# Kernel optimization log

Hardware: AMD Instinct MI355X
Metric: run time of the kernel (lower is better)

## Reference

```python
import jax, jax.numpy as jnp
import numpy as np
from jax import lax

N_QUBITS = 8
N_BLOCKS = 5

_H = jnp.array([[1.0, 1.0], [1.0, -1.0]], dtype=jnp.complex64) / np.sqrt(2.0).astype(np.float32)
# torchquantum PauliY.diagonalizing_gates = [Z, S, H] applied in order -> matrix H @ S @ Z = H @ diag(1, -1j)
_YROT = _H @ jnp.diag(jnp.array([1.0, -1j], dtype=jnp.complex64))


def apply_gate(st, U, wires):
    # st: [N, 2, 2, ..., 2] (n_qubits trailing axes); U: [2^k, 2^k]
    k = len(wires)
    axes = [w + 1 for w in wires]
    s = jnp.moveaxis(st, axes, list(range(1, k + 1)))
    shp = s.shape
    s = s.reshape(shp[0], 2 ** k, -1)
    s = jnp.einsum('ij,bjr->bir', U, s)
    return jnp.moveaxis(s.reshape(shp), list(range(1, k + 1)), axes)


def u3_mat(th, ph, lam):
    c = jnp.cos(0.5 * th).astype(jnp.complex64)
    s = jnp.sin(0.5 * th).astype(jnp.complex64)
    el = jnp.exp(1j * lam)
    ep = jnp.exp(1j * ph)
    return jnp.stack([jnp.stack([c, -el * s]), jnp.stack([ep * s, ep * el * c])])


def cu3_mat(th, ph, lam):
    M = jnp.eye(4, dtype=jnp.complex64)
    return M.at[2:, 2:].set(u3_mat(th, ph, lam))


def z_expvals(st):
    # <Z_w> for every wire from marginal probabilities
    n = st.ndim - 1
    mag = st.real ** 2 + st.imag ** 2
    outs = []
    for w in range(n):
        axes = tuple(a for a in range(1, n + 1) if a != w + 1)
        p = mag.sum(axes)  # [N, 2]
        outs.append(p[:, 0] - p[:, 1])
    return jnp.stack(outs, axis=1)


def quantum_conv(x, conv_w, conv_b, u3_params, cu3_params, fc_w, fc_b):
    n = N_QUBITS
    B, C, H, W = x.shape
    y = lax.conv_general_dilated(x, conv_w, (1, 1), 'SAME',
                                 dimension_numbers=('NCHW', 'OIHW', 'NCHW'))
    y = y + conv_b[None, :, None, None]
    ang = y.transpose(0, 2, 3, 1).reshape(-1, n)  # [B*H*W, n_qubits]
    Npx = ang.shape[0]
    # RY(theta)|0> encoding: product state of [cos(t/2), sin(t/2)] per wire
    c = jnp.cos(0.5 * ang)
    s = jnp.sin(0.5 * ang)
    st = jnp.stack([c[:, 0], s[:, 0]], axis=1).astype(jnp.complex64)
    for w in range(1, n):
        q = jnp.stack([c[:, w], s[:, w]], axis=1).astype(jnp.complex64)
        st = (st[:, :, None] * q[:, None, :]).reshape(Npx, -1)
    st = st.reshape((Npx,) + (2,) * n)
    # U3CU3Layer0: per block, U3 on each wire then circular CU3 ring
    for b in range(N_BLOCKS):
        for w in range(n):
            st = apply_gate(st, u3_mat(u3_params[b, w, 0], u3_params[b, w, 1], u3_params[b, w, 2]), [w])
        for w in range(n):
            st = apply_gate(st, cu3_mat(cu3_params[b, w, 0], cu3_params[b, w, 1], cu3_params[b, w, 2]), [w, (w + 1) % n])
    # MeasureAll(Z), then MeasureAll(X) and MeasureAll(Y) which MUTATE the device
    # state with their diagonalizing gates (torchquantum semantics)
    mz = z_expvals(st)
    for w in range(n):
        st = apply_gate(st, _H, [w])
    mx = z_expvals(st)
    for w in range(n):
        st = apply_gate(st, _YROT, [w])
    my = z_expvals(st)
    meas = jnp.concatenate([mz, mx, my], axis=1)  # [B*H*W, 3*n]
    out = meas @ fc_w.T + fc_b
    return out.reshape(B, H, W, -1).transpose(0, 3, 1, 2)


def setup_inputs() -> dict:
    key = jax.random.key(0)
    ks = jax.random.split(key, 7)
    n, cin, cout = N_QUBITS, 16, 32
    x = jax.random.normal(ks[0], (4, cin, 64, 64), dtype=jnp.float32)
    conv_w = jax.random.normal(ks[1], (n, cin, 3, 3), dtype=jnp.float32) / np.sqrt(cin * 9)
    conv_b = jax.random.normal(ks[2], (n,), dtype=jnp.float32) * 0.01
    u3_params = jax.random.uniform(ks[3], (N_BLOCKS, n, 3), dtype=jnp.float32, minval=-np.pi, maxval=np.pi)
    cu3_params = jax.random.uniform(ks[4], (N_BLOCKS, n, 3), dtype=jnp.float32, minval=-np.pi, maxval=np.pi)
    fc_w = jax.random.normal(ks[5], (cout, 3 * n), dtype=jnp.float32) / np.sqrt(3 * n)
    fc_b = jax.random.normal(ks[6], (cout,), dtype=jnp.float32) * 0.01
    return {'x': x, 'conv_w': conv_w, 'conv_b': conv_b, 'u3_params': u3_params,
            'cu3_params': cu3_params, 'fc_w': fc_w, 'fc_b': fc_b}


def reference(x, conv_w, conv_b, u3_params, cu3_params, fc_w, fc_b):
    return quantum_conv(x, conv_w, conv_b, u3_params, cu3_params, fc_w, fc_b)
```

## Files before the change

kernel.cpp:

```cpp
#include <hip/hip_runtime.h>

typedef float v2f __attribute__((ext_vector_type(2)));

template<int C>
__device__ __forceinline__ float dppmov(float x) {
  return __int_as_float(__builtin_amdgcn_update_dpp(0, __float_as_int(x), C, 0xF, 0xF, true));
}
template<int IMM>
__device__ __forceinline__ float dswz(float x) {
  return __int_as_float(__builtin_amdgcn_ds_swizzle(__float_as_int(x), IMM));
}
__device__ __forceinline__ float bperm(float x, int a) {
  return __int_as_float(__builtin_amdgcn_ds_bpermute(a, __float_as_int(x)));
}
template<int M>
__device__ __forceinline__ float bfly(float x) {
  if constexpr (M == 1)      return dppmov<0xB1>(x);
  else if constexpr (M == 2) return dppmov<0x4E>(x);
  else if constexpr (M == 8) return dppmov<0x128>(x);
  else                       return dswz<0x101F>(x);
}
template<int M>
__device__ __forceinline__ v2f bfly2(v2f v) {
  v2f o; o.x = bfly<M>(v.x); o.y = bfly<M>(v.y); return o;
}
__device__ __forceinline__ v2f sp(float s) { v2f v; v.x = s; v.y = s; return v; }
__device__ __forceinline__ v2f vfma(v2f a, v2f b, v2f c) {
  return __builtin_elementwise_fma(a, b, c);
}

template<int M, int CM>
__device__ __forceinline__ void crossG(v2f Sr[16], v2f Si[16],
    const float* __restrict__ g, int lane) {
  const bool hi = (lane & M) != 0;
  float fr, fi, gr, gi;
  if constexpr (CM == 0) {
    fr = hi ? g[6] : g[0]; fi = hi ? g[7] : g[1];
    gr = hi ? g[4] : g[2]; gi = hi ? g[5] : g[3];
  } else {
    const bool ct = (lane & CM) != 0;
    float f0r = hi ? g[6]  : g[0],  f0i = hi ? g[7]  : g[1];
    float g0r = hi ? g[4]  : g[2],  g0i = hi ? g[5]  : g[3];
    float f1r = hi ? g[14] : g[8],  f1i = hi ? g[15] : g[9];
    float g1r = hi ? g[12] : g[10], g1i = hi ? g[13] : g[11];
    fr = ct ? f1r : f0r; fi = ct ? f1i : f0i;
    gr = ct ? g1r : g0r; gi = ct ? g1i : g0i;
  }
  v2f vfr = sp(fr), vfi = sp(fi), vgr = sp(gr), vgi = sp(gi);
  v2f vfiN = sp(-fi), vgiN = sp(-gi);
#pragma unroll
  for (int r = 0; r < 16; ++r) {
    v2f pR = bfly2<M>(Sr[r]);
    v2f pI = bfly2<M>(Si[r]);
    v2f nR = vfma(vgiN, pI, vfma(vgr, pR, vfma(vfiN, Si[r], vfr * Sr[r])));
    v2f nI = vfma(vgi,  pR, vfma(vgr, pI, vfma(vfi,  Sr[r], vfr * Si[r])));
    Sr[r] = nR; Si[r] = nI;
  }
}

__device__ __forceinline__ void mixP(v2f& x0r, v2f& x0i, v2f& x1r, v2f& x1i,
    float m0r, float m0i, float m1r, float m1i,
    float m2r, float m2i, float m3r, float m3i) {
  v2f n0r = vfma(sp(-m1i), x1i, vfma(sp(m1r), x1r, vfma(sp(-m0i), x0i, sp(m0r) * x0r)));
  v2f n0i = vfma(sp( m1i), x1r, vfma(sp(m1r), x1i, vfma(sp( m0i), x0r, sp(m0r) * x0i)));
  v2f n1r = vfma(sp(-m3i), x1i, vfma(sp(m3r), x1r, vfma(sp(-m2i), x0i, sp(m2r) * x0r)));
  v2f n1i = vfma(sp( m3i), x1r, vfma(sp(m3r), x1i, vfma(sp( m2i), x0r, sp(m2r) * x0i)));
  x0r = n0r; x0i = n0i; x1r = n1r; x1i = n1i;
}

__device__ __forceinline__ void f4N(v2f Sr[16], v2f Si[16],
    const float* __restrict__ g, int lane) {
  const bool ct = (lane & 1) != 0;
  float m[8];
#pragma unroll
  for (int jj = 0; jj < 8; ++jj) m[jj] = ct ? g[8 + jj] : g[jj];
#pragma unroll
  for (int r = 0; r < 8; ++r)
    mixP(Sr[r], Si[r], Sr[r + 8], Si[r + 8],
         m[0], m[1], m[2], m[3], m[4], m[5], m[6], m[7]);
}
__device__ __forceinline__ void f5N(v2f Sr[16], v2f Si[16],
    const float* __restrict__ g) {
#pragma unroll
  for (int r = 0; r < 4; ++r)
    mixP(Sr[r], Si[r], Sr[r + 4], Si[r + 4],
         g[0], g[1], g[2], g[3], g[4], g[5], g[6], g[7]);
#pragma unroll
  for (int r = 8; r < 12; ++r)
    mixP(Sr[r], Si[r], Sr[r + 4], Si[r + 4],
         g[8], g[9], g[10], g[11], g[12], g[13], g[14], g[15]);
}
__device__ __forceinline__ void f6N(v2f Sr[16], v2f Si[16],
    const float* __restrict__ g) {
#pragma unroll
  for (int t = 0; t < 4; ++t) {
    const int r0 = (t >> 1) * 8 + (t & 1);
    mixP(Sr[r0], Si[r0], Sr[r0 + 2], Si[r0 + 2],
         g[0], g[1], g[2], g[3], g[4], g[5], g[6], g[7]);
    const int r1 = r0 + 4;
    mixP(Sr[r1], Si[r1], Sr[r1 + 2], Si[r1 + 2],
         g[8], g[9], g[10], g[11], g[12], g[13], g[14], g[15]);
  }
}
__device__ __forceinline__ void f7N(v2f Sr[16], v2f Si[16],
    const float* __restrict__ g) {
#pragma unroll
  for (int t = 0; t < 4; ++t) {
    const int r0 = t * 4;
    mixP(Sr[r0], Si[r0], Sr[r0 + 1], Si[r0 + 1],
         g[0], g[1], g[2], g[3], g[4], g[5], g[6], g[7]);
    const int r1 = r0 + 2;
    mixP(Sr[r1], Si[r1], Sr[r1 + 1], Si[r1 + 1],
         g[8], g[9], g[10], g[11], g[12], g[13], g[14], g[15]);
  }
}
__device__ __forceinline__ void f8pN(v2f Sr[16], v2f Si[16],
    const float* __restrict__ g, int lane) {
  const bool hi = (lane & 8) != 0;
  float fr[2], fi[2], gr[2], gi[2];
  fr[0] = hi ? g[6]  : g[0];  fi[0] = hi ? g[7]  : g[1];
  gr[0] = hi ? g[4]  : g[2];  gi[0] = hi ? g[5]  : g[3];
  fr[1] = hi ? g[14] : g[8];  fi[1] = hi ? g[15] : g[9];
  gr[1] = hi ? g[12] : g[10]; gi[1] = hi ? g[13] : g[11];
#pragma unroll
  for (int r = 0; r < 16; ++r) {
    const int m = r & 1;
    v2f pR = bfly2<8>(Sr[r]);
    v2f pI = bfly2<8>(Si[r]);
    v2f nR = vfma(sp(-gi[m]), pI, vfma(sp(gr[m]), pR, vfma(sp(-fi[m]), Si[r], sp(fr[m]) * Sr[r])));
    v2f nI = vfma(sp( gi[m]), pR, vfma(sp(gr[m]), pI, vfma(sp( fi[m]), Sr[r], sp(fr[m]) * Si[r])));
    Sr[r] = nR; Si[r] = nI;
  }
}
__device__ __forceinline__ void f8N(v2f Sr[16], v2f Si[16],
    const float* __restrict__ g, int lane) {
  const bool hi = (lane & 8) != 0;
  const float fr = hi ? g[6] : g[0], fi = hi ? g[7] : g[1];
  const float gr = hi ? g[4] : g[2], gi = hi ? g[5] : g[3];
#pragma unroll
  for (int r = 1; r < 16; r += 2) {
    v2f pR = bfly2<8>(Sr[r]);
    v2f pI = bfly2<8>(Si[r]);
    v2f nR = vfma(sp(-gi), pI, vfma(sp(gr), pR, vfma(sp(-fi), Si[r], sp(fr) * Sr[r])));
    v2f nI = vfma(sp( gi), pR, vfma(sp(gr), pI, vfma(sp( fi), Sr[r], sp(fr) * Si[r])));
    Sr[r] = nR; Si[r] = nI;
  }
}

template<int M>
__device__ __forceinline__ void hstepN(v2f Sr[16], v2f Si[16], float sgn) {
  v2f s = sp(sgn);
#pragma unroll
  for (int r = 0; r < 16; ++r) {
    v2f pR = bfly2<M>(Sr[r]);
    v2f pI = bfly2<M>(Si[r]);
    Sr[r] = vfma(s, Sr[r], pR);
    Si[r] = vfma(s, Si[r], pI);
  }
}
__device__ __forceinline__ void hp(v2f& a, v2f& b) { v2f t = a; a = t + b; b = t - b; }
__device__ __forceinline__ void hintraN(v2f S[16]) {
  hp(S[0],S[8]);  hp(S[1],S[9]);  hp(S[2],S[10]); hp(S[3],S[11]);
  hp(S[4],S[12]); hp(S[5],S[13]); hp(S[6],S[14]); hp(S[7],S[15]);
  hp(S[0],S[4]);  hp(S[1],S[5]);  hp(S[2],S[6]);  hp(S[3],S[7]);
  hp(S[8],S[12]); hp(S[9],S[13]); hp(S[10],S[14]); hp(S[11],S[15]);
  hp(S[0],S[2]);  hp(S[1],S[3]);  hp(S[4],S[6]);  hp(S[5],S[7]);
  hp(S[8],S[10]); hp(S[9],S[11]); hp(S[12],S[14]); hp(S[13],S[15]);
  hp(S[0],S[1]);  hp(S[2],S[3]);  hp(S[4],S[5]);  hp(S[6],S[7]);
  hp(S[8],S[9]);  hp(S[10],S[11]); hp(S[12],S[13]); hp(S[14],S[15]);
}
__device__ __forceinline__ void hallN(v2f Sr[16], v2f Si[16], const float* sg) {
  hstepN<8>(Sr, Si, sg[0]);
  hstepN<4>(Sr, Si, sg[1]);
  hstepN<2>(Sr, Si, sg[2]);
  hstepN<1>(Sr, Si, sg[3]);
  hintraN(Sr); hintraN(Si);
}

__device__ __forceinline__ void phaseYN(v2f Sr[16], v2f Si[16], int lane) {
  const int pl = __popc(lane & 15);
#pragma unroll
  for (int r = 0; r < 16; ++r) {
    const int qq = (pl + __popc(r)) & 3;
    const bool b0 = (qq & 1) != 0;
    const bool b1 = (qq & 2) != 0;
    const float sR = b1 ? -1.0f : 1.0f;
    const float sI = (b0 != b1) ? -1.0f : 1.0f;
    v2f Rs = b0 ? Si[r] : Sr[r];
    v2f Is = b0 ? Sr[r] : Si[r];
    Sr[r] = sp(sR) * Rs;
    Si[r] = sp(sI) * Is;
  }
}

__device__ __forceinline__ void measureN(const v2f Sr[16], const v2f Si[16],
    const float* sg, v2f m[8]) {
  v2f P[16];
#pragma unroll
  for (int r = 0; r < 16; ++r) P[r] = vfma(Si[r], Si[r], Sr[r] * Sr[r]);
  v2f t01[8], d7 = sp(0.0f);
#pragma unroll
  for (int jj = 0; jj < 8; ++jj) {
    t01[jj] = P[2 * jj] + P[2 * jj + 1];
    d7 = d7 + (P[2 * jj] - P[2 * jj + 1]);
  }
  v2f d6 = (t01[0] - t01[1]) + (t01[2] - t01[3]) + (t01[4] - t01[5]) + (t01[6] - t01[7]);
  v2f q0 = t01[0] + t01[1], q1 = t01[2] + t01[3];
  v2f q2 = t01[4] + t01[5], q3 = t01[6] + t01[7];
  v2f d5 = (q0 - q1) + (q2 - q3);
  v2f d4 = (q0 + q1) - (q2 + q3);
  v2f pa = (q0 + q1) + (q2 + q3);
  v2f c0 = sp(sg[0]) * pa, c1 = sp(sg[1]) * pa;
  v2f c2 = sp(sg[2]) * pa, c3 = sp(sg[3]) * pa;
  v2f c4 = d4, c5 = d5, c6 = d6, c7 = d7;
#define BSUM(M) \
  c0 = c0 + bfly2<M>(c0); c1 = c1 + bfly2<M>(c1); \
  c2 = c2 + bfly2<M>(c2); c3 = c3 + bfly2<M>(c3); \
  c4 = c4 + bfly2<M>(c4); c5 = c5 + bfly2<M>(c5); \
  c6 = c6 + bfly2<M>(c6); c7 = c7 + bfly2<M>(c7);
  BSUM(1) BSUM(2) BSUM(4) BSUM(8)
#undef BSUM
  m[0] = c0; m[1] = c1; m[2] = c2; m[3] = c3;
  m[4] = c4; m[5] = c5; m[6] = c6; m[7] = c7;
}

__device__ __forceinline__ void fcN(const v2f m[8],
    const float* __restrict__ wbase, bool isB, int j, float acc[4]) {
  float mm[8];
#pragma unroll
  for (int w = 0; w < 8; ++w) mm[w] = isB ? m[w].y : m[w].x;
#pragma unroll
  for (int k = 0; k < 4; ++k) {
    const float4* w4 = reinterpret_cast<const float4*>(wbase + (4 * j + k) * 8);
    float4 a = w4[0], b = w4[1];
    float s = acc[k];
    s = fmaf(mm[0], a.x, s); s = fmaf(mm[1], a.y, s);
    s = fmaf(mm[2], a.z, s); s = fmaf(mm[3], a.w, s);
    s = fmaf(mm[4], b.x, s); s = fmaf(mm[5], b.y, s);
    s = fmaf(mm[6], b.z, s); s = fmaf(mm[7], b.w, s);
    acc[k] = s;
  }
}

__device__ __forceinline__ void mm2(const float* A, const float* B, float* D) {
  D[0] = A[0]*B[0] - A[1]*B[1] + A[2]*B[4] - A[3]*B[5];
  D[1] = A[0]*B[1] + A[1]*B[0] + A[2]*B[5] + A[3]*B[4];
  D[2] = A[0]*B[2] - A[1]*B[3] + A[2]*B[6] - A[3]*B[7];
  D[3] = A[0]*B[3] + A[1]*B[2] + A[2]*B[7] + A[3]*B[6];
  D[4] = A[4]*B[0] - A[5]*B[1] + A[6]*B[4] - A[7]*B[5];
  D[5] = A[4]*B[1] + A[5]*B[0] + A[6]*B[5] + A[7]*B[4];
  D[6] = A[4]*B[2] - A[5]*B[3] + A[6]*B[6] - A[7]*B[7];
  D[7] = A[4]*B[3] + A[5]*B[2] + A[6]*B[7] + A[7]*B[6];
}
__device__ __forceinline__ void u3fill(const float* src, float* o) {
  float th = src[0], ph = src[1], lam = src[2];
  float c = cosf(0.5f * th), s = sinf(0.5f * th);
  float cl = cosf(lam), sl = sinf(lam);
  float cp = cosf(ph), spv = sinf(ph);
  float cpl = cosf(ph + lam), spl = sinf(ph + lam);
  o[0] = c;        o[1] = 0.0f;
  o[2] = -cl * s;  o[3] = -sl * s;
  o[4] = cp * s;   o[5] = spv * s;
  o[6] = cpl * c;  o[7] = spl * c;
}

__global__ __launch_bounds__(128) void prep_kernel(
    const float* __restrict__ u3p, const float* __restrict__ cu3p,
    const float* __restrict__ fcw, float* __restrict__ G,
    float* __restrict__ FCW2) {
  __shared__ float Us[40][8];
  __shared__ float Cs[40][8];
  int t = threadIdx.x;
  if (t < 40) u3fill(u3p + t * 3, Us[t]);
  if (t >= 64 && t < 104) u3fill(cu3p + (t - 64) * 3, Cs[t - 64]);
  __syncthreads();
  if (t == 0) {
#pragma unroll
    for (int j = 0; j < 8; ++j) G[j] = Us[0][j];
  } else if (t < 36) {
    int j = t - 1, b = j / 7, k = j % 7;
    float* dst = G + 8 + b * 112 + k * 16;
    const float* U = Us[b * 8 + k + 1];
    const float* C = Cs[b * 8 + k];
#pragma unroll
    for (int q = 0; q < 8; ++q) dst[q] = U[q];
    mm2(C, U, dst + 8);
  } else if (t < 40) {
    int b = t - 36;
    float* dst = G + 568 + b * 16;
    const float* U = Us[(b + 1) * 8];
    const float* C = Cs[b * 8 + 7];
#pragma unroll
    for (int q = 0; q < 8; ++q) dst[q] = U[q];
    mm2(U, C, dst + 8);
  } else if (t == 40) {
#pragma unroll
    for (int j = 0; j < 8; ++j) G[632 + j] = Cs[39][j];
  }
  for (int i = t; i < 768; i += 128) {
    int s = i >> 8, cc = (i >> 3) & 31, wv = i & 7;
    float sc = (s == 0) ? 1.0f : ((s == 1) ? (1.0f / 256.0f) : (1.0f / 65536.0f));
    FCW2[i] = fcw[cc * 24 + s * 8 + wv] * sc;
  }
}

__global__ __launch_bounds__(256) void qconv_kernel(
    const float* __restrict__ x, const float* __restrict__ cw,
    const float* __restrict__ cb, const float* __restrict__ G,
    const float* __restrict__ FCW2, const float* __restrict__ fcb,
    float* __restrict__ out) {
  const int lane = threadIdx.x & 63;
  const int wid = __builtin_amdgcn_readfirstlane(
      (int)((blockIdx.x * blockDim.x + threadIdx.x) >> 6));
  const int p0 = wid * 8;
  const int q = lane & 15;

  float sg[4];
  sg[0] = (q & 8) ? -1.0f : 1.0f;
  sg[1] = (q & 4) ? -1.0f : 1.0f;
  sg[2] = (q & 2) ? -1.0f : 1.0f;
  sg[3] = (q & 1) ? -1.0f : 1.0f;

  float ang;
  {
    const int px = lane >> 3;
    const int oc = lane & 7;
    const int p  = p0 + px;
    const int b  = p >> 12;
    const int hh = (p >> 6) & 63;
    const int wim = p & 63;
    float acc = cb[oc];
#pragma unroll 4
    for (int ic = 0; ic < 16; ++ic) {
      const float* wp = cw + (oc * 16 + ic) * 9;
      const float* xp = x + (b * 16 + ic) * 4096;
#pragma unroll
      for (int kh = 0; kh < 3; ++kh) {
        int ih = hh + kh - 1;
        bool rok = (unsigned)ih < 64u;
        int ihc = rok ? ih : 0;
#pragma unroll
        for (int kw = 0; kw < 3; ++kw) {
          int iw = wim + kw - 1;
          bool ok = rok && ((unsigned)iw < 64u);
          int iwc = ((unsigned)iw < 64u) ? iw : 0;
          float xv = xp[ihc * 64 + iwc];
          acc = fmaf(ok ? xv : 0.0f, wp[kh * 3 + kw], acc);
        }
      }
    }
    ang = acc;
  }

  v2f Sr[16], Si[16];
  {
    const int gb = (lane & 48) << 2;
    float aA[8], aB[8];
#pragma unroll
    for (int w = 0; w < 8; ++w) {
      aA[w] = bperm(ang, gb + (w << 2));
      aB[w] = bperm(ang, gb + ((8 + w) << 2));
    }
    float cA[8], sA[8], cB[8], sB[8];
#pragma unroll
    for (int w = 0; w < 8; ++w) {
      __sincosf(0.5f * aA[w], &sA[w], &cA[w]);
      __sincosf(0.5f * aB[w], &sB[w], &cB[w]);
    }
    float fA = ((q & 8) ? sA[0] : cA[0]) * ((q & 4) ? sA[1] : cA[1])
             * ((q & 2) ? sA[2] : cA[2]) * ((q & 1) ? sA[3] : cA[3]);
    float fB = ((q & 8) ? sB[0] : cB[0]) * ((q & 4) ? sB[1] : cB[1])
             * ((q & 2) ? sB[2] : cB[2]) * ((q & 1) ? sB[3] : cB[3]);
    v2f uu[4], vv[4];
    uu[0].x = cA[6]*cA[7]; uu[1].x = cA[6]*sA[7];
    uu[2].x = sA[6]*cA[7]; uu[3].x = sA[6]*sA[7];
    uu[0].y = cB[6]*cB[7]; uu[1].y = cB[6]*sB[7];
    uu[2].y = sB[6]*cB[7]; uu[3].y = sB[6]*sB[7];
    float vA0 = fA * cA[4], vA1 = fA * sA[4];
    float vB0 = fB * cB[4], vB1 = fB * sB[4];
    vv[0].x = vA0*cA[5]; vv[1].x = vA0*sA[5];
    vv[2].x = vA1*cA[5]; vv[3].x = vA1*sA[5];
    vv[0].y = vB0*cB[5]; vv[1].y = vB0*sB[5];
    vv[2].y = vB1*cB[5]; vv[3].y = vB1*sB[5];
#pragma unroll
    for (int r = 0; r < 16; ++r) {
      Sr[r] = vv[r >> 2] * uu[r & 3];
      Si[r] = sp(0.0f);
    }
  }

  crossG<8, 0>(Sr, Si, G, lane);
  for (int b = 0; b < 5; ++b) {
    const float* base = G + 8 + b * 112;
    crossG<4, 8>(Sr, Si, base +  0, lane);
    crossG<2, 4>(Sr, Si, base + 16, lane);
    crossG<1, 2>(Sr, Si, base + 32, lane);
    f4N(Sr, Si, base + 48, lane);
    f5N(Sr, Si, base + 64);
    f6N(Sr, Si, base + 80);
    f7N(Sr, Si, base + 96);
    if (b < 4) f8pN(Sr, Si, G + 568 + b * 16, lane);
  }
  f8N(Sr, Si, G + 632, lane);

  const int j = q & 7;
  const bool isB = (q & 8) != 0;
  float acc[4];
#pragma unroll
  for (int k = 0; k < 4; ++k) acc[k] = fcb[4 * j + k];

  v2f m[8];
  measureN(Sr, Si, sg, m);
  fcN(m, FCW2, isB, j, acc);
  hallN(Sr, Si, sg);
  measureN(Sr, Si, sg, m);
  fcN(m, FCW2 + 256, isB, j, acc);
  phaseYN(Sr, Si, lane);
  hallN(Sr, Si, sg);
  measureN(Sr, Si, sg, m);
  fcN(m, FCW2 + 512, isB, j, acc);

  const int g = lane >> 4;
  const int p = p0 + 2 * g + (isB ? 1 : 0);
  const int ob = (p >> 12) * 131072 + (p & 4095);
#pragma unroll
  for (int k = 0; k < 4; ++k)
    out[ob + (4 * j + k) * 4096] = acc[k];
}

extern "C" void kernel_launch(void* const* d_in, const int* in_sizes, int n_in,
                              void* d_out, int out_size, void* d_ws, size_t ws_size,
                              hipStream_t stream) {
  const float* x      = (const float*)d_in[0];
  const float* conv_w = (const float*)d_in[1];
  const float* conv_b = (const float*)d_in[2];
  const float* u3p    = (const float*)d_in[3];
  const float* cu3p   = (const float*)d_in[4];
  const float* fcw    = (const float*)d_in[5];
  const float* fcb    = (const float*)d_in[6];
  float* out = (float*)d_out;

  float* ws   = (float*)d_ws;
  float* G    = ws;
  float* FCW2 = ws + 640;

  prep_kernel<<<1, 128, 0, stream>>>(u3p, cu3p, fcw, G, FCW2);
  qconv_kernel<<<512, 256, 0, stream>>>(x, conv_w, conv_b, G, FCW2, fcb, out);
}
```

Baseline: 112.6 us.

## Spread each statevector across 32 lanes with 8 amplitude pairs per lane

```diff
diff --git a/kernel.cpp b/kernel.cpp
--- a/kernel.cpp
+++ b/kernel.cpp
@@ -15,10 +15,11 @@
 }
 template<int M>
 __device__ __forceinline__ float bfly(float x) {
-  if constexpr (M == 1)      return dppmov<0xB1>(x);
-  else if constexpr (M == 2) return dppmov<0x4E>(x);
-  else if constexpr (M == 8) return dppmov<0x128>(x);
-  else                       return dswz<0x101F>(x);
+  if constexpr (M == 1)       return dppmov<0xB1>(x);
+  else if constexpr (M == 2)  return dppmov<0x4E>(x);
+  else if constexpr (M == 8)  return dppmov<0x128>(x);
+  else if constexpr (M == 4)  return dswz<0x101F>(x);
+  else                        return dswz<0x401F>(x);
 }
 template<int M>
 __device__ __forceinline__ v2f bfly2(v2f v) {
@@ -30,7 +31,7 @@
 }
 
 template<int M, int CM>
-__device__ __forceinline__ void crossG(v2f Sr[16], v2f Si[16],
+__device__ __forceinline__ void crossG(v2f Sr[8], v2f Si[8],
     const float* __restrict__ g, int lane) {
   const bool hi = (lane & M) != 0;
   float fr, fi, gr, gi;
@@ -49,7 +50,7 @@
   v2f vfr = sp(fr), vfi = sp(fi), vgr = sp(gr), vgi = sp(gi);
   v2f vfiN = sp(-fi), vgiN = sp(-gi);
 #pragma unroll
-  for (int r = 0; r < 16; ++r) {
+  for (int r = 0; r < 8; ++r) {
     v2f pR = bfly2<M>(Sr[r]);
     v2f pI = bfly2<M>(Si[r]);
     v2f nR = vfma(vgiN, pI, vfma(vgr, pR, vfma(vfiN, Si[r], vfr * Sr[r])));
@@ -68,79 +69,58 @@
   x0r = n0r; x0i = n0i; x1r = n1r; x1i = n1i;
 }
 
-__device__ __forceinline__ void f4N(v2f Sr[16], v2f Si[16],
+__device__ __forceinline__ void f5N(v2f Sr[8], v2f Si[8],
     const float* __restrict__ g, int lane) {
   const bool ct = (lane & 1) != 0;
   float m[8];
 #pragma unroll
   for (int jj = 0; jj < 8; ++jj) m[jj] = ct ? g[8 + jj] : g[jj];
 #pragma unroll
-  for (int r = 0; r < 8; ++r)
-    mixP(Sr[r], Si[r], Sr[r + 8], Si[r + 8],
-         m[0], m[1], m[2], m[3], m[4], m[5], m[6], m[7]);
-}
-__device__ __forceinline__ void f5N(v2f Sr[16], v2f Si[16],
-    const float* __restrict__ g) {
-#pragma unroll
   for (int r = 0; r < 4; ++r)
     mixP(Sr[r], Si[r], Sr[r + 4], Si[r + 4],
-         g[0], g[1], g[2], g[3], g[4], g[5], g[6], g[7]);
-#pragma unroll
-  for (int r = 8; r < 12; ++r)
-    mixP(Sr[r], Si[r], Sr[r + 4], Si[r + 4],
-         g[8], g[9], g[10], g[11], g[12], g[13], g[14], g[15]);
-}
-__device__ __forceinline__ void f6N(v2f Sr[16], v2f Si[16],
+         m[0], m[1], m[2], m[3], m[4], m[5], m[6], m[7]);
+}
+__device__ __forceinline__ void f6N(v2f Sr[8], v2f Si[8],
     const float* __restrict__ g) {
-#pragma unroll
-  for (int t = 0; t < 4; ++t) {
-    const int r0 = (t >> 1) * 8 + (t & 1);
-    mixP(Sr[r0], Si[r0], Sr[r0 + 2], Si[r0 + 2],
-         g[0], g[1], g[2], g[3], g[4], g[5], g[6], g[7]);
-    const int r1 = r0 + 4;
-    mixP(Sr[r1], Si[r1], Sr[r1 + 2], Si[r1 + 2],
-         g[8], g[9], g[10], g[11], g[12], g[13], g[14], g[15]);
-  }
-}
-__device__ __forceinline__ void f7N(v2f Sr[16], v2f Si[16],
+  mixP(Sr[0], Si[0], Sr[2], Si[2], g[0],g[1],g[2],g[3],g[4],g[5],g[6],g[7]);
+  mixP(Sr[1], Si[1], Sr[3], Si[3], g[0],g[1],g[2],g[3],g[4],g[5],g[6],g[7]);
+  mixP(Sr[4], Si[4], Sr[6], Si[6], g[8],g[9],g[10],g[11],g[12],g[13],g[14],g[15]);
+  mixP(Sr[5], Si[5], Sr[7], Si[7], g[8],g[9],g[10],g[11],g[12],g[13],g[14],g[15]);
+}
+__device__ __forceinline__ void f7N(v2f Sr[8], v2f Si[8],
     const float* __restrict__ g) {
-#pragma unroll
-  for (int t = 0; t < 4; ++t) {
-    const int r0 = t * 4;
-    mixP(Sr[r0], Si[r0], Sr[r0 + 1], Si[r0 + 1],
-         g[0], g[1], g[2], g[3], g[4], g[5], g[6], g[7]);
-    const int r1 = r0 + 2;
-    mixP(Sr[r1], Si[r1], Sr[r1 + 1], Si[r1 + 1],
-         g[8], g[9], g[10], g[11], g[12], g[13], g[14], g[15]);
-  }
-}
-__device__ __forceinline__ void f8pN(v2f Sr[16], v2f Si[16],
+  mixP(Sr[0], Si[0], Sr[1], Si[1], g[0],g[1],g[2],g[3],g[4],g[5],g[6],g[7]);
+  mixP(Sr[4], Si[4], Sr[5], Si[5], g[0],g[1],g[2],g[3],g[4],g[5],g[6],g[7]);
+  mixP(Sr[2], Si[2], Sr[3], Si[3], g[8],g[9],g[10],g[11],g[12],g[13],g[14],g[15]);
+  mixP(Sr[6], Si[6], Sr[7], Si[7], g[8],g[9],g[10],g[11],g[12],g[13],g[14],g[15]);
+}
+__device__ __forceinline__ void f8pN(v2f Sr[8], v2f Si[8],
     const float* __restrict__ g, int lane) {
-  const bool hi = (lane & 8) != 0;
+  const bool hi = (lane & 16) != 0;
   float fr[2], fi[2], gr[2], gi[2];
   fr[0] = hi ? g[6]  : g[0];  fi[0] = hi ? g[7]  : g[1];
   gr[0] = hi ? g[4]  : g[2];  gi[0] = hi ? g[5]  : g[3];
   fr[1] = hi ? g[14] : g[8];  fi[1] = hi ? g[15] : g[9];
   gr[1] = hi ? g[12] : g[10]; gi[1] = hi ? g[13] : g[11];
 #pragma unroll
-  for (int r = 0; r < 16; ++r) {
+  for (int r = 0; r < 8; ++r) {
     const int m = r & 1;
-    v2f pR = bfly2<8>(Sr[r]);
-    v2f pI = bfly2<8>(Si[r]);
+    v2f pR = bfly2<16>(Sr[r]);
+    v2f pI = bfly2<16>(Si[r]);
     v2f nR = vfma(sp(-gi[m]), pI, vfma(sp(gr[m]), pR, vfma(sp(-fi[m]), Si[r], sp(fr[m]) * Sr[r])));
     v2f nI = vfma(sp( gi[m]), pR, vfma(sp(gr[m]), pI, vfma(sp( fi[m]), Sr[r], sp(fr[m]) * Si[r])));
     Sr[r] = nR; Si[r] = nI;
   }
 }
-__device__ __forceinline__ void f8N(v2f Sr[16], v2f Si[16],
+__device__ __forceinline__ void f8N(v2f Sr[8], v2f Si[8],
     const float* __restrict__ g, int lane) {
-  const bool hi = (lane & 8) != 0;
+  const bool hi = (lane & 16) != 0;
   const float fr = hi ? g[6] : g[0], fi = hi ? g[7] : g[1];
   const float gr = hi ? g[4] : g[2], gi = hi ? g[5] : g[3];
 #pragma unroll
-  for (int r = 1; r < 16; r += 2) {
-    v2f pR = bfly2<8>(Sr[r]);
-    v2f pI = bfly2<8>(Si[r]);
+  for (int r = 1; r < 8; r += 2) {
+    v2f pR = bfly2<16>(Sr[r]);
+    v2f pI = bfly2<16>(Si[r]);
     v2f nR = vfma(sp(-gi), pI, vfma(sp(gr), pR, vfma(sp(-fi), Si[r], sp(fr) * Sr[r])));
     v2f nI = vfma(sp( gi), pR, vfma(sp(gr), pI, vfma(sp( fi), Sr[r], sp(fr) * Si[r])));
     Sr[r] = nR; Si[r] = nI;
@@ -148,10 +128,10 @@
 }
 
 template<int M>
-__device__ __forceinline__ void hstepN(v2f Sr[16], v2f Si[16], float sgn) {
+__device__ __forceinline__ void hstepN(v2f Sr[8], v2f Si[8], float sgn) {
   v2f s = sp(sgn);
 #pragma unroll
-  for (int r = 0; r < 16; ++r) {
+  for (int r = 0; r < 8; ++r) {
     v2f pR = bfly2<M>(Sr[r]);
     v2f pI = bfly2<M>(Si[r]);
     Sr[r] = vfma(s, Sr[r], pR);
@@ -159,28 +139,24 @@
   }
 }
 __device__ __forceinline__ void hp(v2f& a, v2f& b) { v2f t = a; a = t + b; b = t - b; }
-__device__ __forceinline__ void hintraN(v2f S[16]) {
-  hp(S[0],S[8]);  hp(S[1],S[9]);  hp(S[2],S[10]); hp(S[3],S[11]);
-  hp(S[4],S[12]); hp(S[5],S[13]); hp(S[6],S[14]); hp(S[7],S[15]);
-  hp(S[0],S[4]);  hp(S[1],S[5]);  hp(S[2],S[6]);  hp(S[3],S[7]);
-  hp(S[8],S[12]); hp(S[9],S[13]); hp(S[10],S[14]); hp(S[11],S[15]);
-  hp(S[0],S[2]);  hp(S[1],S[3]);  hp(S[4],S[6]);  hp(S[5],S[7]);
-  hp(S[8],S[10]); hp(S[9],S[11]); hp(S[12],S[14]); hp(S[13],S[15]);
-  hp(S[0],S[1]);  hp(S[2],S[3]);  hp(S[4],S[5]);  hp(S[6],S[7]);
-  hp(S[8],S[9]);  hp(S[10],S[11]); hp(S[12],S[13]); hp(S[14],S[15]);
-}
-__device__ __forceinline__ void hallN(v2f Sr[16], v2f Si[16], const float* sg) {
-  hstepN<8>(Sr, Si, sg[0]);
-  hstepN<4>(Sr, Si, sg[1]);
-  hstepN<2>(Sr, Si, sg[2]);
-  hstepN<1>(Sr, Si, sg[3]);
+__device__ __forceinline__ void hintraN(v2f S[8]) {
+  hp(S[0],S[4]); hp(S[1],S[5]); hp(S[2],S[6]); hp(S[3],S[7]);
+  hp(S[0],S[2]); hp(S[1],S[3]); hp(S[4],S[6]); hp(S[5],S[7]);
+  hp(S[0],S[1]); hp(S[2],S[3]); hp(S[4],S[5]); hp(S[6],S[7]);
+}
+__device__ __forceinline__ void hallN(v2f Sr[8], v2f Si[8], const float* sg) {
+  hstepN<16>(Sr, Si, sg[0]);
+  hstepN<8>(Sr, Si, sg[1]);
+  hstepN<4>(Sr, Si, sg[2]);
+  hstepN<2>(Sr, Si, sg[3]);
+  hstepN<1>(Sr, Si, sg[4]);
   hintraN(Sr); hintraN(Si);
 }
 
-__device__ __forceinline__ void phaseYN(v2f Sr[16], v2f Si[16], int lane) {
-  const int pl = __popc(lane & 15);
-#pragma unroll
-  for (int r = 0; r < 16; ++r) {
+__device__ __forceinline__ void phaseYN(v2f Sr[8], v2f Si[8], int lane) {
+  const int pl = __popc(lane & 31);
+#pragma unroll
+  for (int r = 0; r < 8; ++r) {
     const int qq = (pl + __popc(r)) & 3;
     const bool b0 = (qq & 1) != 0;
     const bool b1 = (qq & 2) != 0;
@@ -193,45 +169,39 @@
   }
 }
 
-__device__ __forceinline__ void measureN(const v2f Sr[16], const v2f Si[16],
+__device__ __forceinline__ void measureN(const v2f Sr[8], const v2f Si[8],
     const float* sg, v2f m[8]) {
-  v2f P[16];
-#pragma unroll
-  for (int r = 0; r < 16; ++r) P[r] = vfma(Si[r], Si[r], Sr[r] * Sr[r]);
-  v2f t01[8], d7 = sp(0.0f);
-#pragma unroll
-  for (int jj = 0; jj < 8; ++jj) {
-    t01[jj] = P[2 * jj] + P[2 * jj + 1];
-    d7 = d7 + (P[2 * jj] - P[2 * jj + 1]);
-  }
-  v2f d6 = (t01[0] - t01[1]) + (t01[2] - t01[3]) + (t01[4] - t01[5]) + (t01[6] - t01[7]);
-  v2f q0 = t01[0] + t01[1], q1 = t01[2] + t01[3];
-  v2f q2 = t01[4] + t01[5], q3 = t01[6] + t01[7];
-  v2f d5 = (q0 - q1) + (q2 - q3);
-  v2f d4 = (q0 + q1) - (q2 + q3);
-  v2f pa = (q0 + q1) + (q2 + q3);
-  v2f c0 = sp(sg[0]) * pa, c1 = sp(sg[1]) * pa;
-  v2f c2 = sp(sg[2]) * pa, c3 = sp(sg[3]) * pa;
-  v2f c4 = d4, c5 = d5, c6 = d6, c7 = d7;
+  v2f P[8];
+#pragma unroll
+  for (int r = 0; r < 8; ++r) P[r] = vfma(Si[r], Si[r], Sr[r] * Sr[r]);
+  v2f d7 = (P[0] - P[1]) + (P[2] - P[3]) + (P[4] - P[5]) + (P[6] - P[7]);
+  v2f t0 = P[0] + P[1], t1 = P[2] + P[3], t2 = P[4] + P[5], t3 = P[6] + P[7];
+  v2f d6 = (t0 - t1) + (t2 - t3);
+  v2f q0 = t0 + t1, q1 = t2 + t3;
+  v2f d5 = q0 - q1;
+  v2f pa = q0 + q1;
+  v2f c0 = sp(sg[0]) * pa, c1 = sp(sg[1]) * pa, c2 = sp(sg[2]) * pa;
+  v2f c3 = sp(sg[3]) * pa, c4 = sp(sg[4]) * pa;
+  v2f c5 = d5, c6 = d6, c7 = d7;
 #define BSUM(M) \
   c0 = c0 + bfly2<M>(c0); c1 = c1 + bfly2<M>(c1); \
   c2 = c2 + bfly2<M>(c2); c3 = c3 + bfly2<M>(c3); \
   c4 = c4 + bfly2<M>(c4); c5 = c5 + bfly2<M>(c5); \
   c6 = c6 + bfly2<M>(c6); c7 = c7 + bfly2<M>(c7);
-  BSUM(1) BSUM(2) BSUM(4) BSUM(8)
+  BSUM(1) BSUM(2) BSUM(4) BSUM(8) BSUM(16)
 #undef BSUM
   m[0] = c0; m[1] = c1; m[2] = c2; m[3] = c3;
   m[4] = c4; m[5] = c5; m[6] = c6; m[7] = c7;
 }
 
 __device__ __forceinline__ void fcN(const v2f m[8],
-    const float* __restrict__ wbase, bool isB, int j, float acc[4]) {
+    const float* __restrict__ wbase, bool isB, int j, float acc[2]) {
   float mm[8];
 #pragma unroll
   for (int w = 0; w < 8; ++w) mm[w] = isB ? m[w].y : m[w].x;
 #pragma unroll
-  for (int k = 0; k < 4; ++k) {
-    const float4* w4 = reinterpret_cast<const float4*>(wbase + (4 * j + k) * 8);
+  for (int k = 0; k < 2; ++k) {
+    const float4* w4 = reinterpret_cast<const float4*>(wbase + (2 * j + k) * 8);
     float4 a = w4[0], b = w4[1];
     float s = acc[k];
     s = fmaf(mm[0], a.x, s); s = fmaf(mm[1], a.y, s);
@@ -312,26 +282,29 @@
   const int lane = threadIdx.x & 63;
   const int wid = __builtin_amdgcn_readfirstlane(
       (int)((blockIdx.x * blockDim.x + threadIdx.x) >> 6));
-  const int p0 = wid * 8;
-  const int q = lane & 15;
-
-  float sg[4];
-  sg[0] = (q & 8) ? -1.0f : 1.0f;
-  sg[1] = (q & 4) ? -1.0f : 1.0f;
-  sg[2] = (q & 2) ? -1.0f : 1.0f;
-  sg[3] = (q & 1) ? -1.0f : 1.0f;
+  const int p0 = wid * 4;
+  const int q = lane & 31;
+
+  float sg[5];
+  sg[0] = (q & 16) ? -1.0f : 1.0f;
+  sg[1] = (q & 8)  ? -1.0f : 1.0f;
+  sg[2] = (q & 4)  ? -1.0f : 1.0f;
+  sg[3] = (q & 2)  ? -1.0f : 1.0f;
+  sg[4] = (q & 1)  ? -1.0f : 1.0f;
 
   float ang;
   {
-    const int px = lane >> 3;
-    const int oc = lane & 7;
-    const int p  = p0 + px;
-    const int b  = p >> 12;
-    const int hh = (p >> 6) & 63;
+    const int icg = lane & 1;
+    const int oc  = (lane >> 1) & 7;
+    const int px  = lane >> 4;
+    const int p   = p0 + px;
+    const int b   = p >> 12;
+    const int hh  = (p >> 6) & 63;
     const int wim = p & 63;
-    float acc = cb[oc];
-#pragma unroll 4
-    for (int ic = 0; ic < 16; ++ic) {
+    float acc = 0.0f;
+#pragma unroll 2
+    for (int il = 0; il < 8; ++il) {
+      const int ic = icg * 8 + il;
       const float* wp = cw + (oc * 16 + ic) * 9;
       const float* xp = x + (b * 16 + ic) * 4096;
 #pragma unroll
@@ -349,17 +322,18 @@
         }
       }
     }
-    ang = acc;
-  }
-
-  v2f Sr[16], Si[16];
+    acc += bfly<1>(acc);
+    ang = acc + cb[oc];
+  }
+
+  v2f Sr[8], Si[8];
   {
-    const int gb = (lane & 48) << 2;
+    const int gb = lane & 32;
     float aA[8], aB[8];
 #pragma unroll
     for (int w = 0; w < 8; ++w) {
-      aA[w] = bperm(ang, gb + (w << 2));
-      aB[w] = bperm(ang, gb + ((8 + w) << 2));
+      aA[w] = bperm(ang, (gb + 2 * w) << 2);
+      aB[w] = bperm(ang, (gb + 16 + 2 * w) << 2);
     }
     float cA[8], sA[8], cB[8], sB[8];
 #pragma unroll
@@ -367,47 +341,45 @@
       __sincosf(0.5f * aA[w], &sA[w], &cA[w]);
       __sincosf(0.5f * aB[w], &sB[w], &cB[w]);
     }
-    float fA = ((q & 8) ? sA[0] : cA[0]) * ((q & 4) ? sA[1] : cA[1])
-             * ((q & 2) ? sA[2] : cA[2]) * ((q & 1) ? sA[3] : cA[3]);
-    float fB = ((q & 8) ? sB[0] : cB[0]) * ((q & 4) ? sB[1] : cB[1])
-             * ((q & 2) ? sB[2] : cB[2]) * ((q & 1) ? sB[3] : cB[3]);
-    v2f uu[4], vv[4];
+    float fA = ((q & 16) ? sA[0] : cA[0]) * ((q & 8) ? sA[1] : cA[1])
+             * ((q & 4) ? sA[2] : cA[2]) * ((q & 2) ? sA[3] : cA[3])
+             * ((q & 1) ? sA[4] : cA[4]);
+    float fB = ((q & 16) ? sB[0] : cB[0]) * ((q & 8) ? sB[1] : cB[1])
+             * ((q & 4) ? sB[2] : cB[2]) * ((q & 2) ? sB[3] : cB[3])
+             * ((q & 1) ? sB[4] : cB[4]);
+    v2f uu[4], vv[2];
     uu[0].x = cA[6]*cA[7]; uu[1].x = cA[6]*sA[7];
     uu[2].x = sA[6]*cA[7]; uu[3].x = sA[6]*sA[7];
     uu[0].y = cB[6]*cB[7]; uu[1].y = cB[6]*sB[7];
     uu[2].y = sB[6]*cB[7]; uu[3].y = sB[6]*sB[7];
-    float vA0 = fA * cA[4], vA1 = fA * sA[4];
-    float vB0 = fB * cB[4], vB1 = fB * sB[4];
-    vv[0].x = vA0*cA[5]; vv[1].x = vA0*sA[5];
-    vv[2].x = vA1*cA[5]; vv[3].x = vA1*sA[5];
-    vv[0].y = vB0*cB[5]; vv[1].y = vB0*sB[5];
-    vv[2].y = vB1*cB[5]; vv[3].y = vB1*sB[5];
-#pragma unroll
-    for (int r = 0; r < 16; ++r) {
+    vv[0].x = fA * cA[5]; vv[1].x = fA * sA[5];
+    vv[0].y = fB * cB[5]; vv[1].y = fB * sB[5];
+#pragma unroll
+    for (int r = 0; r < 8; ++r) {
       Sr[r] = vv[r >> 2] * uu[r & 3];
       Si[r] = sp(0.0f);
     }
   }
 
-  crossG<8, 0>(Sr, Si, G, lane);
+  crossG<16, 0>(Sr, Si, G, lane);
   for (int b = 0; b < 5; ++b) {
     const float* base = G + 8 + b * 112;
-    crossG<4, 8>(Sr, Si, base +  0, lane);
-    crossG<2, 4>(Sr, Si, base + 16, lane);
-    crossG<1, 2>(Sr, Si, base + 32, lane);
-    f4N(Sr, Si, base + 48, lane);
-    f5N(Sr, Si, base + 64);
+    crossG<8, 16>(Sr, Si, base +  0, lane);
+    crossG<4, 8> (Sr, Si, base + 16, lane);
+    crossG<2, 4> (Sr, Si, base + 32, lane);
+    crossG<1, 2> (Sr, Si, base + 48, lane);
+    f5N(Sr, Si, base + 64, lane);
     f6N(Sr, Si, base + 80);
     f7N(Sr, Si, base + 96);
     if (b < 4) f8pN(Sr, Si, G + 568 + b * 16, lane);
   }
   f8N(Sr, Si, G + 632, lane);
 
-  const int j = q & 7;
-  const bool isB = (q & 8) != 0;
-  float acc[4];
-#pragma unroll
-  for (int k = 0; k < 4; ++k) acc[k] = fcb[4 * j + k];
+  const int j = q & 15;
+  const bool isB = (q & 16) != 0;
+  float acc[2];
+  acc[0] = fcb[2 * j];
+  acc[1] = fcb[2 * j + 1];
 
   v2f m[8];
   measureN(Sr, Si, sg, m);
@@ -420,12 +392,11 @@
   measureN(Sr, Si, sg, m);
   fcN(m, FCW2 + 512, isB, j, acc);
 
-  const int g = lane >> 4;
+  const int g = lane >> 5;
   const int p = p0 + 2 * g + (isB ? 1 : 0);
   const int ob = (p >> 12) * 131072 + (p & 4095);
-#pragma unroll
-  for (int k = 0; k < 4; ++k)
-    out[ob + (4 * j + k) * 4096] = acc[k];
+  out[ob + (2 * j) * 4096]     = acc[0];
+  out[ob + (2 * j + 1) * 4096] = acc[1];
 }
 
 extern "C" void kernel_launch(void* const* d_in, const int* in_sizes, int n_in,
@@ -445,5 +416,5 @@
   float* FCW2 = ws + 640;
 
   prep_kernel<<<1, 128, 0, stream>>>(u3p, cu3p, fcw, G, FCW2);
-  qconv_kernel<<<512, 256, 0, stream>>>(x, conv_w, conv_b, G, FCW2, fcb, out);
-}
+  qconv_kernel<<<1024, 256, 0, stream>>>(x, conv_w, conv_b, G, FCW2, fcb, out);
+}
```

Result: slower. 119.1 us (+5.8%).

## Compute X/Y expectations via pairwise amplitude products instead of basis rotations

Applied to the files above, without the earlier changes.

```diff
diff --git a/kernel.cpp b/kernel.cpp
--- a/kernel.cpp
+++ b/kernel.cpp
@@ -148,98 +148,19 @@
 }
 
 template<int M>
-__device__ __forceinline__ void hstepN(v2f Sr[16], v2f Si[16], float sgn) {
-  v2f s = sp(sgn);
-#pragma unroll
-  for (int r = 0; r < 16; ++r) {
-    v2f pR = bfly2<M>(Sr[r]);
-    v2f pI = bfly2<M>(Si[r]);
-    Sr[r] = vfma(s, Sr[r], pR);
-    Si[r] = vfma(s, Si[r], pI);
-  }
-}
-__device__ __forceinline__ void hp(v2f& a, v2f& b) { v2f t = a; a = t + b; b = t - b; }
-__device__ __forceinline__ void hintraN(v2f S[16]) {
-  hp(S[0],S[8]);  hp(S[1],S[9]);  hp(S[2],S[10]); hp(S[3],S[11]);
-  hp(S[4],S[12]); hp(S[5],S[13]); hp(S[6],S[14]); hp(S[7],S[15]);
-  hp(S[0],S[4]);  hp(S[1],S[5]);  hp(S[2],S[6]);  hp(S[3],S[7]);
-  hp(S[8],S[12]); hp(S[9],S[13]); hp(S[10],S[14]); hp(S[11],S[15]);
-  hp(S[0],S[2]);  hp(S[1],S[3]);  hp(S[4],S[6]);  hp(S[5],S[7]);
-  hp(S[8],S[10]); hp(S[9],S[11]); hp(S[12],S[14]); hp(S[13],S[15]);
-  hp(S[0],S[1]);  hp(S[2],S[3]);  hp(S[4],S[5]);  hp(S[6],S[7]);
-  hp(S[8],S[9]);  hp(S[10],S[11]); hp(S[12],S[13]); hp(S[14],S[15]);
-}
-__device__ __forceinline__ void hallN(v2f Sr[16], v2f Si[16], const float* sg) {
-  hstepN<8>(Sr, Si, sg[0]);
-  hstepN<4>(Sr, Si, sg[1]);
-  hstepN<2>(Sr, Si, sg[2]);
-  hstepN<1>(Sr, Si, sg[3]);
-  hintraN(Sr); hintraN(Si);
-}
-
-__device__ __forceinline__ void phaseYN(v2f Sr[16], v2f Si[16], int lane) {
-  const int pl = __popc(lane & 15);
-#pragma unroll
-  for (int r = 0; r < 16; ++r) {
-    const int qq = (pl + __popc(r)) & 3;
-    const bool b0 = (qq & 1) != 0;
-    const bool b1 = (qq & 2) != 0;
-    const float sR = b1 ? -1.0f : 1.0f;
-    const float sI = (b0 != b1) ? -1.0f : 1.0f;
-    v2f Rs = b0 ? Si[r] : Sr[r];
-    v2f Is = b0 ? Sr[r] : Si[r];
-    Sr[r] = sp(sR) * Rs;
-    Si[r] = sp(sI) * Is;
-  }
-}
-
-__device__ __forceinline__ void measureN(const v2f Sr[16], const v2f Si[16],
-    const float* sg, v2f m[8]) {
-  v2f P[16];
-#pragma unroll
-  for (int r = 0; r < 16; ++r) P[r] = vfma(Si[r], Si[r], Sr[r] * Sr[r]);
-  v2f t01[8], d7 = sp(0.0f);
-#pragma unroll
-  for (int jj = 0; jj < 8; ++jj) {
-    t01[jj] = P[2 * jj] + P[2 * jj + 1];
-    d7 = d7 + (P[2 * jj] - P[2 * jj + 1]);
-  }
-  v2f d6 = (t01[0] - t01[1]) + (t01[2] - t01[3]) + (t01[4] - t01[5]) + (t01[6] - t01[7]);
-  v2f q0 = t01[0] + t01[1], q1 = t01[2] + t01[3];
-  v2f q2 = t01[4] + t01[5], q3 = t01[6] + t01[7];
-  v2f d5 = (q0 - q1) + (q2 - q3);
-  v2f d4 = (q0 + q1) - (q2 + q3);
-  v2f pa = (q0 + q1) + (q2 + q3);
-  v2f c0 = sp(sg[0]) * pa, c1 = sp(sg[1]) * pa;
-  v2f c2 = sp(sg[2]) * pa, c3 = sp(sg[3]) * pa;
-  v2f c4 = d4, c5 = d5, c6 = d6, c7 = d7;
-#define BSUM(M) \
-  c0 = c0 + bfly2<M>(c0); c1 = c1 + bfly2<M>(c1); \
-  c2 = c2 + bfly2<M>(c2); c3 = c3 + bfly2<M>(c3); \
-  c4 = c4 + bfly2<M>(c4); c5 = c5 + bfly2<M>(c5); \
-  c6 = c6 + bfly2<M>(c6); c7 = c7 + bfly2<M>(c7);
-  BSUM(1) BSUM(2) BSUM(4) BSUM(8)
-#undef BSUM
-  m[0] = c0; m[1] = c1; m[2] = c2; m[3] = c3;
-  m[4] = c4; m[5] = c5; m[6] = c6; m[7] = c7;
-}
-
-__device__ __forceinline__ void fcN(const v2f m[8],
-    const float* __restrict__ wbase, bool isB, int j, float acc[4]) {
-  float mm[8];
-#pragma unroll
-  for (int w = 0; w < 8; ++w) mm[w] = isB ? m[w].y : m[w].x;
-#pragma unroll
-  for (int k = 0; k < 4; ++k) {
-    const float4* w4 = reinterpret_cast<const float4*>(wbase + (4 * j + k) * 8);
-    float4 a = w4[0], b = w4[1];
-    float s = acc[k];
-    s = fmaf(mm[0], a.x, s); s = fmaf(mm[1], a.y, s);
-    s = fmaf(mm[2], a.z, s); s = fmaf(mm[3], a.w, s);
-    s = fmaf(mm[4], b.x, s); s = fmaf(mm[5], b.y, s);
-    s = fmaf(mm[6], b.z, s); s = fmaf(mm[7], b.w, s);
-    acc[k] = s;
-  }
+__device__ __forceinline__ void crossO(const v2f Sr[16], const v2f Si[16],
+                                       v2f& re, v2f& im) {
+  v2f r = sp(0.0f), i = sp(0.0f);
+#pragma unroll
+  for (int k = 0; k < 16; ++k) {
+    v2f pr = bfly2<M>(Sr[k]);
+    v2f pi = bfly2<M>(Si[k]);
+    r = vfma(Sr[k], pr, r);
+    r = vfma(Si[k], pi, r);
+    i = vfma(Si[k], pr, i);
+    i = vfma(-Sr[k], pi, i);
+  }
+  re = r; im = i;
 }
 
 __device__ __forceinline__ void mm2(const float* A, const float* B, float* D) {
@@ -267,7 +188,7 @@
 __global__ __launch_bounds__(128) void prep_kernel(
     const float* __restrict__ u3p, const float* __restrict__ cu3p,
     const float* __restrict__ fcw, float* __restrict__ G,
-    float* __restrict__ FCW2) {
+    float* __restrict__ FCW3) {
   __shared__ float Us[40][8];
   __shared__ float Cs[40][8];
   int t = threadIdx.x;
@@ -298,28 +219,23 @@
     for (int j = 0; j < 8; ++j) G[632 + j] = Cs[39][j];
   }
   for (int i = t; i < 768; i += 128) {
-    int s = i >> 8, cc = (i >> 3) & 31, wv = i & 7;
-    float sc = (s == 0) ? 1.0f : ((s == 1) ? (1.0f / 256.0f) : (1.0f / 65536.0f));
-    FCW2[i] = fcw[cc * 24 + s * 8 + wv] * sc;
+    int tt = i % 24;
+    int stage = tt >> 3, w = tt & 7;
+    float sc = (stage >= 1 && w >= 4) ? 2.0f : 1.0f;
+    FCW3[i] = fcw[i] * sc;
   }
 }
 
 __global__ __launch_bounds__(256) void qconv_kernel(
     const float* __restrict__ x, const float* __restrict__ cw,
     const float* __restrict__ cb, const float* __restrict__ G,
-    const float* __restrict__ FCW2, const float* __restrict__ fcb,
+    const float* __restrict__ FCW3, const float* __restrict__ fcb,
     float* __restrict__ out) {
   const int lane = threadIdx.x & 63;
   const int wid = __builtin_amdgcn_readfirstlane(
       (int)((blockIdx.x * blockDim.x + threadIdx.x) >> 6));
   const int p0 = wid * 8;
   const int q = lane & 15;
-
-  float sg[4];
-  sg[0] = (q & 8) ? -1.0f : 1.0f;
-  sg[1] = (q & 4) ? -1.0f : 1.0f;
-  sg[2] = (q & 2) ? -1.0f : 1.0f;
-  sg[3] = (q & 1) ? -1.0f : 1.0f;
 
   float ang;
   {
@@ -367,10 +283,19 @@
       __sincosf(0.5f * aA[w], &sA[w], &cA[w]);
       __sincosf(0.5f * aB[w], &sB[w], &cB[w]);
     }
-    float fA = ((q & 8) ? sA[0] : cA[0]) * ((q & 4) ? sA[1] : cA[1])
-             * ((q & 2) ? sA[2] : cA[2]) * ((q & 1) ? sA[3] : cA[3]);
-    float fB = ((q & 8) ? sB[0] : cB[0]) * ((q & 4) ? sB[1] : cB[1])
-             * ((q & 2) ? sB[2] : cB[2]) * ((q & 1) ? sB[3] : cB[3]);
+    v2f c0; c0.x = cA[0]; c0.y = cB[0];
+    v2f s0; s0.x = sA[0]; s0.y = sB[0];
+    v2f c0r = vfma(sp(G[2]), s0, sp(G[0]) * c0);
+    v2f c0i = vfma(sp(G[3]), s0, sp(G[1]) * c0);
+    v2f s0r = vfma(sp(G[6]), s0, sp(G[4]) * c0);
+    v2f s0i = vfma(sp(G[7]), s0, sp(G[5]) * c0);
+    const bool w0 = (q & 8) != 0;
+    v2f selR = w0 ? s0r : c0r;
+    v2f selI = w0 ? s0i : c0i;
+    float fA = ((q & 4) ? sA[1] : cA[1]) * ((q & 2) ? sA[2] : cA[2])
+             * ((q & 1) ? sA[3] : cA[3]);
+    float fB = ((q & 4) ? sB[1] : cB[1]) * ((q & 2) ? sB[2] : cB[2])
+             * ((q & 1) ? sB[3] : cB[3]);
     v2f uu[4], vv[4];
     uu[0].x = cA[6]*cA[7]; uu[1].x = cA[6]*sA[7];
     uu[2].x = sA[6]*cA[7]; uu[3].x = sA[6]*sA[7];
@@ -384,12 +309,12 @@
     vv[2].y = vB1*cB[5]; vv[3].y = vB1*sB[5];
 #pragma unroll
     for (int r = 0; r < 16; ++r) {
-      Sr[r] = vv[r >> 2] * uu[r & 3];
-      Si[r] = sp(0.0f);
-    }
-  }
-
-  crossG<8, 0>(Sr, Si, G, lane);
+      v2f base = vv[r >> 2] * uu[r & 3];
+      Sr[r] = selR * base;
+      Si[r] = selI * base;
+    }
+  }
+
   for (int b = 0; b < 5; ++b) {
     const float* base = G + 8 + b * 112;
     crossG<4, 8>(Sr, Si, base +  0, lane);
@@ -403,29 +328,107 @@
   }
   f8N(Sr, Si, G + 632, lane);
 
+  float sg[4];
+  sg[0] = (q & 8) ? -1.0f : 1.0f;
+  sg[1] = (q & 4) ? -1.0f : 1.0f;
+  sg[2] = (q & 2) ? -1.0f : 1.0f;
+  sg[3] = (q & 1) ? -1.0f : 1.0f;
+
+  v2f PT[24];
+  {
+    v2f re0, im0, re1, im1, re2, im2, re3, im3;
+    crossO<8>(Sr, Si, re0, im0);
+    crossO<4>(Sr, Si, re1, im1);
+    crossO<2>(Sr, Si, re2, im2);
+    crossO<1>(Sr, Si, re3, im3);
+    PT[8]  = re0; PT[9]  = re1; PT[10] = re2; PT[11] = re3;
+    PT[16] = sp(sg[0]) * im0; PT[17] = sp(sg[1]) * im1;
+    PT[18] = sp(sg[2]) * im2; PT[19] = sp(sg[3]) * im3;
+
+    v2f P[16];
+#pragma unroll
+    for (int r = 0; r < 16; ++r) P[r] = vfma(Si[r], Si[r], Sr[r] * Sr[r]);
+    v2f t01[8];
+#pragma unroll
+    for (int k = 0; k < 8; ++k) t01[k] = P[2*k] + P[2*k+1];
+    v2f q0 = t01[0] + t01[1], q1 = t01[2] + t01[3];
+    v2f q2 = t01[4] + t01[5], q3 = t01[6] + t01[7];
+    v2f h0 = q0 + q1, h1 = q2 + q3;
+    v2f p  = h0 + h1;
+    PT[4] = h0 - h1;
+    PT[5] = (q0 - q1) + (q2 - q3);
+    PT[6] = (t01[0]-t01[1]) + (t01[2]-t01[3])
+          + (t01[4]-t01[5]) + (t01[6]-t01[7]);
+    PT[7] = (P[0]-P[1]) + (P[2]-P[3]) + (P[4]-P[5]) + (P[6]-P[7])
+          + (P[8]-P[9]) + (P[10]-P[11]) + (P[12]-P[13]) + (P[14]-P[15]);
+    PT[0] = sp(sg[0]) * p; PT[1] = sp(sg[1]) * p;
+    PT[2] = sp(sg[2]) * p; PT[3] = sp(sg[3]) * p;
+
+    v2f re, im;
+    re = sp(0.0f); im = sp(0.0f);
+#pragma unroll
+    for (int r = 0; r < 8; ++r) {
+      re = vfma(Sr[r], Sr[r+8], re); re = vfma(Si[r], Si[r+8], re);
+      im = vfma(Si[r], Sr[r+8], im); im = vfma(-Sr[r], Si[r+8], im);
+    }
+    PT[12] = re; PT[20] = im;
+    re = sp(0.0f); im = sp(0.0f);
+#pragma unroll
+    for (int t = 0; t < 8; ++t) {
+      const int lo = (t & 3) + (t >> 2) * 8;
+      re = vfma(Sr[lo], Sr[lo+4], re); re = vfma(Si[lo], Si[lo+4], re);
+      im = vfma(Si[lo], Sr[lo+4], im); im = vfma(-Sr[lo], Si[lo+4], im);
+    }
+    PT[13] = re; PT[21] = im;
+    re = sp(0.0f); im = sp(0.0f);
+#pragma unroll
+    for (int t = 0; t < 8; ++t) {
+      const int lo = (t & 1) + (t >> 1) * 4;
+      re = vfma(Sr[lo], Sr[lo+2], re); re = vfma(Si[lo], Si[lo+2], re);
+      im = vfma(Si[lo], Sr[lo+2], im); im = vfma(-Sr[lo], Si[lo+2], im);
+    }
+    PT[14] = re; PT[22] = im;
+    re = sp(0.0f); im = sp(0.0f);
+#pragma unroll
+    for (int t = 0; t < 8; ++t) {
+      const int lo = 2 * t;
+      re = vfma(Sr[lo], Sr[lo+1], re); re = vfma(Si[lo], Si[lo+1], re);
+      im = vfma(Si[lo], Sr[lo+1], im); im = vfma(-Sr[lo], Si[lo+1], im);
+    }
+    PT[15] = re; PT[23] = im;
+  }
+
   const int j = q & 7;
   const bool isB = (q & 8) != 0;
-  float acc[4];
-#pragma unroll
-  for (int k = 0; k < 4; ++k) acc[k] = fcb[4 * j + k];
-
-  v2f m[8];
-  measureN(Sr, Si, sg, m);
-  fcN(m, FCW2, isB, j, acc);
-  hallN(Sr, Si, sg);
-  measureN(Sr, Si, sg, m);
-  fcN(m, FCW2 + 256, isB, j, acc);
-  phaseYN(Sr, Si, lane);
-  hallN(Sr, Si, sg);
-  measureN(Sr, Si, sg, m);
-  fcN(m, FCW2 + 512, isB, j, acc);
+  float mm[24];
+#pragma unroll
+  for (int t = 0; t < 24; ++t) {
+    v2f v = PT[t] + bfly2<8>(PT[t]);
+    float s = isB ? v.y : v.x;
+    s += bfly<1>(s);
+    s += bfly<2>(s);
+    s += bfly<4>(s);
+    mm[t] = s;
+  }
 
   const int g = lane >> 4;
   const int p = p0 + 2 * g + (isB ? 1 : 0);
   const int ob = (p >> 12) * 131072 + (p & 4095);
 #pragma unroll
-  for (int k = 0; k < 4; ++k)
-    out[ob + (4 * j + k) * 4096] = acc[k];
+  for (int k = 0; k < 4; ++k) {
+    const int ch = 4 * j + k;
+    const float4* w4 = reinterpret_cast<const float4*>(FCW3 + ch * 24);
+    float acc = fcb[ch];
+#pragma unroll
+    for (int u = 0; u < 6; ++u) {
+      float4 tv = w4[u];
+      acc = fmaf(mm[u*4+0], tv.x, acc);
+      acc = fmaf(mm[u*4+1], tv.y, acc);
+      acc = fmaf(mm[u*4+2], tv.z, acc);
+      acc = fmaf(mm[u*4+3], tv.w, acc);
+    }
+    out[ob + ch * 4096] = acc;
+  }
 }
 
 extern "C" void kernel_launch(void* const* d_in, const int* in_sizes, int n_in,
@@ -442,8 +445,8 @@
 
   float* ws   = (float*)d_ws;
   float* G    = ws;
-  float* FCW2 = ws + 640;
-
-  prep_kernel<<<1, 128, 0, stream>>>(u3p, cu3p, fcw, G, FCW2);
-  qconv_kernel<<<512, 256, 0, stream>>>(x, conv_w, conv_b, G, FCW2, fcb, out);
-}
+  float* FCW3 = ws + 640;
+
+  prep_kernel<<<1, 128, 0, stream>>>(u3p, cu3p, fcw, G, FCW3);
+  qconv_kernel<<<512, 256, 0, stream>>>(x, conv_w, conv_b, G, FCW3, fcb, out);
+}
```

After: 114.5 us. Within noise of the previous version (+1.6%).
